# Optimization experiments

Hardware: AMD Instinct MI355X
Metric: run time of the kernel (lower is better)

## Reference

```python
import jax, jax.numpy as jnp
import numpy as np

D = 256
H = 4
HD = D // H


def rotate_half(x):
    xp = x.reshape(x.shape[:-1] + (-1, 2))
    x1, x2 = xp[..., 0], xp[..., 1]
    return jnp.stack((-x2, x1), axis=-1).reshape(x.shape)


def apply_rope(freqs, t):
    # freqs: [2, B, 1, N, HD]; t: [B, H, N, HD]
    return t * freqs[0] + rotate_half(t) * freqs[1]


def layernorm(x, g, b, eps=1e-5):
    m = jnp.mean(x, axis=-1, keepdims=True)
    v = jnp.var(x, axis=-1, keepdims=True)
    return (x - m) * jax.lax.rsqrt(v + eps) * g + b


def ffn(z, W1, b1, g, be, W2, b2):
    h = layernorm(z @ W1 + b1, g, be)
    h = jax.nn.gelu(h, approximate=False)
    return h @ W2 + b2


def heads_split(t):
    B, N, _ = t.shape
    return t.reshape(B, N, H, HD).transpose(0, 2, 1, 3)  # [B,H,N,HD]


def heads_merge(t):
    B, h, N, hd = t.shape
    return t.transpose(0, 2, 1, 3).reshape(B, N, h * hd)


def sdpa(q, k, v):
    s = q.shape[-1] ** (-0.5)
    sim = jnp.einsum('bhid,bhjd->bhij', q, k) * s
    attn = jax.nn.softmax(sim, axis=-1)
    return jnp.einsum('bhij,bhjd->bhid', attn, v)


def self_block(x, enc, Wqkv, bqkv, Wo, bo, W1, b1, g, be, W2, b2):
    B, N, _ = x.shape
    qkv = (x @ Wqkv + bqkv).reshape(B, N, H, HD, 3).transpose(0, 2, 1, 3, 4)
    q, k, v = qkv[..., 0], qkv[..., 1], qkv[..., 2]
    q = apply_rope(enc, q)
    k = apply_rope(enc, k)
    msg = heads_merge(sdpa(q, k, v)) @ Wo + bo
    return x + ffn(jnp.concatenate([x, msg], axis=-1), W1, b1, g, be, W2, b2)


def cross_block(x0, x1, Wqk, bqk, Wv, bv, Wo, bo, W1, b1, g, be, W2, b2):
    qk0 = heads_split(x0 @ Wqk + bqk)
    qk1 = heads_split(x1 @ Wqk + bqk)
    v0 = heads_split(x0 @ Wv + bv)
    v1 = heads_split(x1 @ Wv + bv)
    s = HD ** (-0.5)
    qk0 = qk0 * (s ** 0.5)
    qk1 = qk1 * (s ** 0.5)
    sim = jnp.einsum('bhid,bhjd->bhij', qk0, qk1)
    attn01 = jax.nn.softmax(sim, axis=-1)
    attn10 = jax.nn.softmax(sim.transpose(0, 1, 3, 2), axis=-1)
    m0 = jnp.einsum('bhij,bhjd->bhid', attn01, v1)
    m1 = jnp.einsum('bhij,bhjd->bhid', attn10, v0)
    m0 = heads_merge(m0) @ Wo + bo
    m1 = heads_merge(m1) @ Wo + bo
    x0 = x0 + ffn(jnp.concatenate([x0, m0], axis=-1), W1, b1, g, be, W2, b2)
    x1 = x1 + ffn(jnp.concatenate([x1, m1], axis=-1), W1, b1, g, be, W2, b2)
    return x0, x1


def setup_inputs() -> dict:
    key = jax.random.key(0)
    ks = jax.random.split(key, 24)
    B, N = 4, 2048
    desc0 = jax.random.normal(ks[0], (B, N, D), jnp.float32)
    desc1 = jax.random.normal(ks[1], (B, N, D), jnp.float32)
    encoding0 = jax.random.uniform(ks[2], (2, B, 1, N, HD), jnp.float32)
    encoding1 = jax.random.uniform(ks[3], (2, B, 1, N, HD), jnp.float32)

    def lin(k, fin, fout):
        k1, k2 = jax.random.split(k)
        W = jax.random.normal(k1, (fin, fout), jnp.float32) * (fin ** -0.5)
        b = jax.random.normal(k2, (fout,), jnp.float32) * 0.01
        return W, b

    Wqkv, bqkv = lin(ks[4], D, 3 * D)
    Wo_s, bo_s = lin(ks[5], D, D)
    W1_s, b1_s = lin(ks[6], 2 * D, 2 * D)
    g_s = jnp.ones((2 * D,), jnp.float32)
    be_s = jnp.zeros((2 * D,), jnp.float32)
    W2_s, b2_s = lin(ks[7], 2 * D, D)
    Wqk_c, bqk_c = lin(ks[8], D, D)
    Wv_c, bv_c = lin(ks[9], D, D)
    Wo_c, bo_c = lin(ks[10], D, D)
    W1_c, b1_c = lin(ks[11], 2 * D, 2 * D)
    g_c = jnp.ones((2 * D,), jnp.float32)
    be_c = jnp.zeros((2 * D,), jnp.float32)
    W2_c, b2_c = lin(ks[12], 2 * D, D)
    return dict(desc0=desc0, desc1=desc1, encoding0=encoding0, encoding1=encoding1,
                Wqkv=Wqkv, bqkv=bqkv, Wo_s=Wo_s, bo_s=bo_s,
                W1_s=W1_s, b1_s=b1_s, g_s=g_s, be_s=be_s, W2_s=W2_s, b2_s=b2_s,
                Wqk_c=Wqk_c, bqk_c=bqk_c, Wv_c=Wv_c, bv_c=bv_c, Wo_c=Wo_c, bo_c=bo_c,
                W1_c=W1_c, b1_c=b1_c, g_c=g_c, be_c=be_c, W2_c=W2_c, b2_c=b2_c)


def reference(desc0, desc1, encoding0, encoding1,
              Wqkv, bqkv, Wo_s, bo_s, W1_s, b1_s, g_s, be_s, W2_s, b2_s,
              Wqk_c, bqk_c, Wv_c, bv_c, Wo_c, bo_c, W1_c, b1_c, g_c, be_c, W2_c, b2_c):
    d0 = self_block(desc0, encoding0, Wqkv, bqkv, Wo_s, bo_s, W1_s, b1_s, g_s, be_s, W2_s, b2_s)
    d1 = self_block(desc1, encoding1, Wqkv, bqkv, Wo_s, bo_s, W1_s, b1_s, g_s, be_s, W2_s, b2_s)
    return cross_block(d0, d1, Wqk_c, bqk_c, Wv_c, bv_c, Wo_c, bo_c, W1_c, b1_c, g_c, be_c, W2_c, b2_c)
```

## Files before the change

kernel.cpp:

```cpp
#include <hip/hip_runtime.h>
#include <math.h>

#define BB 4
#define HH 4
#define NN 2048
#define DD 256
#define HDIM 64
#define NTOK 8192
#define NTOK2 16384

typedef __attribute__((ext_vector_type(8))) __bf16 bf16x8;
typedef __attribute__((ext_vector_type(8))) unsigned short ushort8;
typedef __attribute__((ext_vector_type(4))) float floatx4;
typedef __attribute__((ext_vector_type(4))) short short4v;

union U8 { ushort8 u; bf16x8 b; };
union U4 { unsigned int u[2]; unsigned long long l; short4v s; };

#define MFMA16(a, b, c) __builtin_amdgcn_mfma_f32_16x16x16bf16_1k(a, b, c, 0, 0, 0)

__device__ __forceinline__ unsigned short f2bf(float x) {
    unsigned int u = __float_as_uint(x);
    u += 0x7FFF + ((u >> 16) & 1);
    return (unsigned short)(u >> 16);
}
__device__ __forceinline__ float bf2f(unsigned short u) {
    return __uint_as_float(((unsigned int)u) << 16);
}
__device__ __forceinline__ unsigned int pkbf(float a, float b) {
    return ((__float_as_uint(a) + 0x8000u) >> 16) |
           ((__float_as_uint(b) + 0x8000u) & 0xFFFF0000u);
}

struct WTab {
    const float* w[7];
    unsigned short* o[7];
    int K[7];
    int N[7];
    int st[7];
    int t0[8];
};

__global__ __launch_bounds__(256) void wtrans(WTab tab)
{
    __shared__ float lds[32][33];
    const int t = threadIdx.x;
    int bid = blockIdx.x;
    int s = 0;
    while (bid >= tab.t0[s + 1]) s++;
    const int ti = bid - tab.t0[s];
    const int K = tab.K[s], N = tab.N[s], st = tab.st[s];
    const int tx = ti % (N / 32), ty = ti / (N / 32);
    const int k0 = ty * 32, n0 = tx * 32;
    const float* W = tab.w[s];
    unsigned short* Wt = tab.o[s];

    {
        int r = t >> 3, c = (t & 7) * 4;
        float4 a = *(const float4*)&W[(size_t)(k0 + r) * N + n0 + c];
        lds[r][c] = a.x; lds[r][c+1] = a.y; lds[r][c+2] = a.z; lds[r][c+3] = a.w;
    }
    __syncthreads();
    {
        int n = t >> 3, kq = (t & 7) * 4;
        ushort4 p;
        p.x = f2bf(lds[kq+0][n]); p.y = f2bf(lds[kq+1][n]);
        p.z = f2bf(lds[kq+2][n]); p.w = f2bf(lds[kq+3][n]);
        *(ushort4*)&Wt[(size_t)(n0 + n) * st + k0 + kq] = p;
    }
}

__global__ __launch_bounds__(256) void wfuse(
    const float* __restrict__ Wo_s, const float* __restrict__ W1_s,
    unsigned short* __restrict__ o_s,
    const float* __restrict__ Wo_c, const float* __restrict__ W1_c,
    unsigned short* __restrict__ o_c)
{
    __shared__ float wo[32][33];
    __shared__ float w1[32][68];
    const int t = threadIdx.x;
    const int bid = blockIdx.x;
    const int seg = bid >> 6, ti_ = bid & 63;
    const int i0 = (ti_ >> 3) * 32, n0 = (ti_ & 7) * 64;
    const float* Wo  = seg ? Wo_c : Wo_s;
    const float* W1b = (seg ? W1_c : W1_s) + 256 * 512;
    unsigned short* out = seg ? o_c : o_s;
    const int ti = t >> 3, tn = t & 7;

    float acc[8] = {};
    for (int jc = 0; jc < 256; jc += 32) {
        {
            int r = t >> 3, c = (t & 7) * 4;
            *(float4*)&wo[r][c] = *(const float4*)&Wo[(size_t)(i0 + r) * 256 + jc + c];
            int c8 = (t & 7) * 8;
            *(float4*)&w1[r][c8]     = *(const float4*)&W1b[(size_t)(jc + r) * 512 + n0 + c8];
            *(float4*)&w1[r][c8 + 4] = *(const float4*)&W1b[(size_t)(jc + r) * 512 + n0 + c8 + 4];
        }
        __syncthreads();
        #pragma unroll
        for (int j = 0; j < 32; j++) {
            float a = wo[ti][j];
            #pragma unroll
            for (int e = 0; e < 8; e++) acc[e] += a * w1[j][tn * 8 + e];
        }
        __syncthreads();
    }
    #pragma unroll
    for (int e = 0; e < 8; e++)
        out[(size_t)(n0 + tn * 8 + e) * 512 + 256 + i0 + ti] = f2bf(acc[e]);
}

__global__ __launch_bounds__(256) void bfuse(
    const float* bo_s, const float* W1_s, const float* b1_s, float* bs,
    const float* bo_c, const float* W1_c, const float* b1_c, float* bc)
{
    const int seg = blockIdx.x >> 1, half = blockIdx.x & 1;
    const int n = half * 256 + threadIdx.x;
    const float* bo  = seg ? bo_c : bo_s;
    const float* W1b = (seg ? W1_c : W1_s) + 256 * 512;
    const float* b1  = seg ? b1_c : b1_s;
    float* out       = seg ? bc : bs;
    float a = b1[n];
    for (int j = 0; j < 256; j++) a += bo[j] * W1b[(size_t)j * 512 + n];
    out[n] = a;
}

__global__ __launch_bounds__(256) void gemm_mfma(
    const unsigned short* __restrict__ A, int lda,
    const unsigned short* __restrict__ Wt, int K,
    const float* __restrict__ bias, const float* __restrict__ bias2, int mode,
    float* outF, unsigned short* outH0, unsigned short* outH1,
    unsigned short* outH2,
    int ldc, const float* R0, const float* R1)
{
    __shared__ __align__(16) unsigned short As[64 * 40];
    __shared__ __align__(16) unsigned short Bs[128 * 40];
    const int t = threadIdx.x;
    const int w = t >> 6, lane = t & 63, quad = lane >> 4, l15 = lane & 15;
    const int m0 = blockIdx.y * 64, n0 = blockIdx.x * 128;
    const int wn = w * 32;
    const int sar = t >> 2, sac = (t & 3) * 8;
    const int sbr = t >> 1, sbc = (t & 1) * 16;

    const unsigned short* Ap = A  + (size_t)(m0 + sar) * lda + sac;
    const unsigned short* Bp = Wt + (size_t)(n0 + sbr) * K   + sbc;

    ushort8 pa  = *(const ushort8*)(Ap);
    ushort8 pb0 = *(const ushort8*)(Bp);
    ushort8 pb1 = *(const ushort8*)(Bp + 8);

    floatx4 acc[4][2];
    #pragma unroll
    for (int i = 0; i < 4; i++)
        #pragma unroll
        for (int j = 0; j < 2; j++) acc[i][j] = (floatx4){0.f, 0.f, 0.f, 0.f};

    const int nk = K >> 5;
    for (int kk = 0; kk < nk; kk++) {
        *(ushort8*)&As[sar * 40 + sac]     = pa;
        *(ushort8*)&Bs[sbr * 40 + sbc]     = pb0;
        *(ushort8*)&Bs[sbr * 40 + sbc + 8] = pb1;
        __syncthreads();
        if (kk + 1 < nk) {
            int ko = (kk + 1) * 32;
            pa  = *(const ushort8*)(Ap + ko);
            pb0 = *(const ushort8*)(Bp + ko);
            pb1 = *(const ushort8*)(Bp + ko + 8);
        }
        U8 af[4], bf[2];
        #pragma unroll
        for (int i = 0; i < 4; i++)
            af[i].u = *(const ushort8*)&As[(i * 16 + l15) * 40 + quad * 8];
        #pragma unroll
        for (int j = 0; j < 2; j++)
            bf[j].u = *(const ushort8*)&Bs[(wn + j * 16 + l15) * 40 + quad * 8];
        #pragma unroll
        for (int i = 0; i < 4; i++)
            #pragma unroll
            for (int j = 0; j < 2; j++)
                acc[i][j] = __builtin_amdgcn_mfma_f32_16x16x32_bf16(af[i].b, bf[j].b, acc[i][j], 0, 0, 0);
        __syncthreads();
    }

    #pragma unroll
    for (int i = 0; i < 4; i++) {
        #pragma unroll
        for (int j = 0; j < 2; j++) {
            int col = n0 + wn + j * 16 + l15;
            float bv = (mode == 2 && col >= 256) ? bias2[col & 255] : bias[col];
            #pragma unroll
            for (int r = 0; r < 4; r++) {
                int grow = m0 + i * 16 + quad * 4 + r;
                float v = acc[i][j][r] + bv;
                if (mode == 1) {
                    outH0[(size_t)grow * ldc + col] = f2bf(v);
                } else if (mode == 2) {
                    int cc = col & 255;
                    int h = cc >> 6, d = cc & 63;
                    int ds = grow >> 13, b = (grow >> 11) & 3, n = grow & 2047;
                    int bh = ds * 16 + b * 4 + h;
                    if (col < 256)
                        outH0[((size_t)bh * NN + n) * HDIM + d] = f2bf(v);
                    else
                        outH1[((size_t)bh * HDIM + d) * NN + n] = f2bf(v);
                } else if (mode == 3) {
                    int sel = col % 3, cc = col / 3;
                    int h = cc >> 6, d = cc & 63;
                    int ds = grow >> 13, b = (grow >> 11) & 3, n = grow & 2047;
                    int bh = ds * 16 + b * 4 + h;
                    if (sel == 0)
                        outH0[((size_t)bh * NN + n) * HDIM + d] = f2bf(v);
                    else if (sel == 1)
                        outH1[((size_t)bh * NN + n) * HDIM + d] = f2bf(v);
                    else
                        outH2[((size_t)bh * HDIM + d) * NN + n] = f2bf(v);
                } else {
                    const float* R = (grow < NTOK) ? R0 : R1;
                    float vv = v + R[(size_t)(grow & 8191) * 256 + col];
                    outF[(size_t)grow * 256 + col] = vv;
                    if (outH0) outH0[(size_t)grow * 256 + col] = f2bf(vv);
                    if (outH1) outH1[(size_t)grow * 512 + col] = f2bf(vv);
                }
            }
        }
    }
}

__global__ __launch_bounds__(256) void rope_k(unsigned short* __restrict__ qb,
                                              unsigned short* __restrict__ kb,
                                              const float* __restrict__ enc0,
                                              const float* __restrict__ enc1)
{
    int i = blockIdx.x * 256 + threadIdx.x;
    int dp = (i & 31) * 2;
    int n  = (i >> 5) & (NN - 1);
    int h  = (i >> 16) & 3;
    int b  = (i >> 18) & 3;
    int ds = (i >> 20) & 1;
    int bf = (i >> 21) & 1;
    unsigned short* tq = (bf ? kb : qb) +
        (((size_t)(ds * 16 + b * 4 + h)) * NN + n) * HDIM + dp;
    const float* e0 = (ds ? enc1 : enc0) + ((size_t)b * NN + n) * HDIM + dp;
    const float* e1 = e0 + (size_t)BB * NN * HDIM;
    float x0 = bf2f(tq[0]), x1 = bf2f(tq[1]);
    float y0 = x0 * e0[0] - x1 * e1[0];
    float y1 = x1 * e0[1] + x0 * e1[1];
    tq[0] = f2bf(y0); tq[1] = f2bf(y1);
}

__global__ __launch_bounds__(256) void flash_attn(
    const unsigned short* __restrict__ Q, const unsigned short* __restrict__ K,
    const unsigned short* __restrict__ V, unsigned short* __restrict__ O,
    int ldo, int kvx, float qscale)
{
    __shared__ __align__(16) unsigned short Ks[64 * 72];
    __shared__ __align__(16) unsigned short Vt[64 * 72];

    const int t    = threadIdx.x;
    const int w    = t >> 6;
    const int lane = t & 63;
    const int quad = lane >> 4;
    const int l15  = lane & 15;
    const int bh   = blockIdx.y;
    const int kbh  = bh ^ kvx;
    const int q0   = blockIdx.x * 64;

    const unsigned short* Qb  = Q + (size_t)bh  * NN * HDIM;
    const unsigned short* Kb  = K + (size_t)kbh * NN * HDIM;
    const unsigned short* VTb = V + (size_t)kbh * NN * HDIM;

    const int srf = t >> 3, scf = (t & 7) * 8;

    const int qrow = q0 + w * 16 + l15;
    bf16x8 qf0, qf1;
    {
        U8 r0, r1, x0, x1;
        r0.u = *(const ushort8*)&Qb[(size_t)qrow * HDIM + quad * 8];
        r1.u = *(const ushort8*)&Qb[(size_t)qrow * HDIM + 32 + quad * 8];
        #pragma unroll
        for (int j = 0; j < 8; j++) {
            x0.u[j] = f2bf(bf2f(r0.u[j]) * qscale);
            x1.u[j] = f2bf(bf2f(r1.u[j]) * qscale);
        }
        qf0 = x0.b; qf1 = x1.b;
    }

    floatx4 o[4];
    #pragma unroll
    for (int c = 0; c < 4; c++) o[c] = (floatx4){0.f, 0.f, 0.f, 0.f};
    float m = -1e30f, l = 0.f;

    ushort8 ka0 = *(const ushort8*)&Kb[(size_t)srf * HDIM + scf];
    ushort8 ka1 = *(const ushort8*)&Kb[(size_t)(srf + 32) * HDIM + scf];
    ushort8 va0 = *(const ushort8*)&VTb[(size_t)srf * NN + scf];
    ushort8 va1 = *(const ushort8*)&VTb[(size_t)(srf + 32) * NN + scf];

    for (int j0 = 0; j0 < NN; j0 += 64) {
        *(ushort8*)&Ks[srf * 72 + scf]        = ka0;
        *(ushort8*)&Ks[(srf + 32) * 72 + scf] = ka1;
        *(ushort8*)&Vt[srf * 72 + scf]        = va0;
        *(ushort8*)&Vt[(srf + 32) * 72 + scf] = va1;
        __syncthreads();
        if (j0 + 64 < NN) {
            int jn = j0 + 64;
            ka0 = *(const ushort8*)&Kb[(size_t)(jn + srf) * HDIM + scf];
            ka1 = *(const ushort8*)&Kb[(size_t)(jn + srf + 32) * HDIM + scf];
            va0 = *(const ushort8*)&VTb[(size_t)srf * NN + jn + scf];
            va1 = *(const ushort8*)&VTb[(size_t)(srf + 32) * NN + jn + scf];
        }

        floatx4 s[4];
        #pragma unroll
        for (int t4 = 0; t4 < 4; t4++) {
            U8 k0, k1;
            k0.u = *(const ushort8*)&Ks[(t4 * 16 + l15) * 72 + quad * 8];
            k1.u = *(const ushort8*)&Ks[(t4 * 16 + l15) * 72 + 32 + quad * 8];
            floatx4 z = (floatx4){0.f, 0.f, 0.f, 0.f};
            z = __builtin_amdgcn_mfma_f32_16x16x32_bf16(k0.b, qf0, z, 0, 0, 0);
            z = __builtin_amdgcn_mfma_f32_16x16x32_bf16(k1.b, qf1, z, 0, 0, 0);
            s[t4] = z;
        }

        float mx = s[0][0];
        #pragma unroll
        for (int t4 = 0; t4 < 4; t4++)
            #pragma unroll
            for (int r = 0; r < 4; r++) mx = fmaxf(mx, s[t4][r]);
        mx = fmaxf(mx, __shfl_xor(mx, 16, 64));
        mx = fmaxf(mx, __shfl_xor(mx, 32, 64));
        float mn = fmaxf(m, mx);
        float al = exp2f(m - mn);
        m = mn;
        float rs = 0.f;
        #pragma unroll
        for (int t4 = 0; t4 < 4; t4++)
            #pragma unroll
            for (int r = 0; r < 4; r++) {
                float p = exp2f(s[t4][r] - mn);
                s[t4][r] = p;
                rs += p;
            }
        rs += __shfl_xor(rs, 16, 64);
        rs += __shfl_xor(rs, 32, 64);
        l = l * al + rs;
        #pragma unroll
        for (int c = 0; c < 4; c++)
            #pragma unroll
            for (int r = 0; r < 4; r++) o[c][r] *= al;

        short4v pf[4];
        #pragma unroll
        for (int t4 = 0; t4 < 4; t4++) {
            U4 pk;
            pk.u[0] = pkbf(s[t4][0], s[t4][1]);
            pk.u[1] = pkbf(s[t4][2], s[t4][3]);
            pf[t4] = pk.s;
        }

        #pragma unroll
        for (int c = 0; c < 4; c++) {
            #pragma unroll
            for (int t4 = 0; t4 < 4; t4++) {
                U4 vf;
                vf.l = *(const unsigned long long*)
                    &Vt[(c * 16 + l15) * 72 + t4 * 16 + quad * 4];
                o[c] = MFMA16(vf.s, pf[t4], o[c]);
            }
        }
        __syncthreads();
    }

    const int ds = bh >> 4, b = (bh >> 2) & 3, h = bh & 3;
    const int q = q0 + w * 16 + l15;
    const size_t row = (size_t)ds * NTOK + b * NN + q;
    float inv = 1.f / l;
    #pragma unroll
    for (int c = 0; c < 4; c++) {
        ushort4 pk;
        pk.x = f2bf(o[c][0] * inv);
        pk.y = f2bf(o[c][1] * inv);
        pk.z = f2bf(o[c][2] * inv);
        pk.w = f2bf(o[c][3] * inv);
        *(ushort4*)&O[row * ldo + h * HDIM + c * 16 + quad * 4] = pk;
    }
}

__global__ __launch_bounds__(256) void ln_gelu(
    unsigned short* __restrict__ hb, const float* __restrict__ g,
    const float* __restrict__ be)
{
    __shared__ float r1[4], r2[4];
    const int t = threadIdx.x;
    const size_t row = blockIdx.x;
    unsigned short* ip = hb + row * 512;
    float x0 = bf2f(ip[t]), x1 = bf2f(ip[t + 256]);
    float s = x0 + x1, ss = x0 * x0 + x1 * x1;
    #pragma unroll
    for (int o = 32; o > 0; o >>= 1) { s += __shfl_down(s, o); ss += __shfl_down(ss, o); }
    if ((t & 63) == 0) { r1[t >> 6] = s; r2[t >> 6] = ss; }
    __syncthreads();
    float S  = r1[0] + r1[1] + r1[2] + r1[3];
    float SS = r2[0] + r2[1] + r2[2] + r2[3];
    float mean = S * (1.f / 512.f);
    float var  = SS * (1.f / 512.f) - mean * mean;
    float inv  = rsqrtf(var + 1e-5f);
    float y0 = (x0 - mean) * inv * g[t]       + be[t];
    float y1 = (x1 - mean) * inv * g[t + 256] + be[t + 256];
    ip[t]       = f2bf(0.5f * y0 * (1.f + erff(y0 * 0.70710678f)));
    ip[t + 256] = f2bf(0.5f * y1 * (1.f + erff(y1 * 0.70710678f)));
}

__global__ __launch_bounds__(256) void copy_to_cat(
    const float* __restrict__ s0, const float* __restrict__ s1,
    unsigned short* __restrict__ cat)
{
    int i = blockIdx.x * 256 + threadIdx.x;
    int row = i >> 6, c4 = (i & 63) * 4;
    const float* s = (row < NTOK) ? s0 : s1;
    float4 a = *(const float4*)&s[(size_t)(row & 8191) * 256 + c4];
    ushort4 p = { f2bf(a.x), f2bf(a.y), f2bf(a.z), f2bf(a.w) };
    *(ushort4*)&cat[(size_t)row * 512 + c4] = p;
}

extern "C" void kernel_launch(void* const* d_in, const int* in_sizes, int n_in,
                              void* d_out, int out_size, void* d_ws, size_t ws_size,
                              hipStream_t stream)
{
    const float* desc0 = (const float*)d_in[0];
    const float* desc1 = (const float*)d_in[1];
    const float* enc0  = (const float*)d_in[2];
    const float* enc1  = (const float*)d_in[3];
    const float* Wqkv  = (const float*)d_in[4];  const float* bqkv  = (const float*)d_in[5];
    const float* Wo_s  = (const float*)d_in[6];  const float* bo_s  = (const float*)d_in[7];
    const float* W1_s  = (const float*)d_in[8];  const float* b1_s  = (const float*)d_in[9];
    const float* g_s   = (const float*)d_in[10]; const float* be_s  = (const float*)d_in[11];
    const float* W2_s  = (const float*)d_in[12]; const float* b2_s  = (const float*)d_in[13];
    const float* Wqk_c = (const float*)d_in[14]; const float* bqk_c = (const float*)d_in[15];
    const float* Wv_c  = (const float*)d_in[16]; const float* bv_c  = (const float*)d_in[17];
    const float* Wo_c  = (const float*)d_in[18]; const float* bo_c  = (const float*)d_in[19];
    const float* W1_c  = (const float*)d_in[20]; const float* b1_c  = (const float*)d_in[21];
    const float* g_c   = (const float*)d_in[22]; const float* be_c  = (const float*)d_in[23];
    const float* W2_c  = (const float*)d_in[24]; const float* b2_c  = (const float*)d_in[25];

    char* ws = (char*)d_ws;
    unsigned short* wt  = (unsigned short*)ws;
    unsigned short* qb  = (unsigned short*)(ws + 2490368);
    unsigned short* kb  = (unsigned short*)(ws + 10878976);
    unsigned short* vb  = (unsigned short*)(ws + 27656192);
    unsigned short* cat = (unsigned short*)(ws + 36044800);
    unsigned short* hb  = (unsigned short*)(ws + 52822016);
    unsigned short* dbf = (unsigned short*)(ws + 86376448);

    unsigned short* t_qkv  = wt;
    float*          bias_s = (float*)(wt + 196608);
    unsigned short* t_w1s  = wt + 262144;
    unsigned short* t_w2s  = wt + 524288;
    unsigned short* t_wqkc = wt + 655360;
    float*          bias_c = (float*)(wt + 786432);
    unsigned short* t_w1c  = wt + 851968;
    unsigned short* t_w2c  = wt + 1114112;

    float* outF = (float*)d_out;

    dim3 blk(256);

    WTab tab;
    tab.w[0] = Wqkv;  tab.o[0] = t_qkv;          tab.K[0] = 256; tab.N[0] = 768; tab.st[0] = 256;
    tab.w[1] = W1_s;  tab.o[1] = t_w1s;          tab.K[1] = 256; tab.N[1] = 512; tab.st[1] = 512;
    tab.w[2] = W2_s;  tab.o[2] = t_w2s;          tab.K[2] = 512; tab.N[2] = 256; tab.st[2] = 512;
    tab.w[3] = Wqk_c; tab.o[3] = t_wqkc;         tab.K[3] = 256; tab.N[3] = 256; tab.st[3] = 256;
    tab.w[4] = Wv_c;  tab.o[4] = t_wqkc + 65536; tab.K[4] = 256; tab.N[4] = 256; tab.st[4] = 256;
    tab.w[5] = W1_c;  tab.o[5] = t_w1c;          tab.K[5] = 256; tab.N[5] = 512; tab.st[5] = 512;
    tab.w[6] = W2_c;  tab.o[6] = t_w2c;          tab.K[6] = 512; tab.N[6] = 256; tab.st[6] = 512;
    int acc_t = 0;
    for (int s = 0; s < 7; s++) {
        tab.t0[s] = acc_t;
        acc_t += (tab.K[s] / 32) * (tab.N[s] / 32);
    }
    tab.t0[7] = acc_t;
    hipLaunchKernelGGL(wtrans, dim3(acc_t), blk, 0, stream, tab);
    hipLaunchKernelGGL(wfuse, dim3(128), blk, 0, stream,
                       Wo_s, W1_s, t_w1s, Wo_c, W1_c, t_w1c);
    hipLaunchKernelGGL(bfuse, dim3(4), blk, 0, stream,
                       bo_s, W1_s, b1_s, bias_s, bo_c, W1_c, b1_c, bias_c);

    auto gemm = [&](const unsigned short* A, int lda, const unsigned short* Wtp,
                    int K, const float* bias, const float* bias2, int Nc, int mode,
                    float* oF, unsigned short* oh0, unsigned short* oh1,
                    unsigned short* oh2, int ldc, const float* r0, const float* r1) {
        dim3 g(Nc / 128, NTOK2 / 64);
        hipLaunchKernelGGL(gemm_mfma, g, blk, 0, stream,
                           A, lda, Wtp, K, bias, bias2, mode,
                           oF, oh0, oh1, oh2, ldc, r0, r1);
    };

    const float QS = 0.125f * 1.44269504088896f;

    hipLaunchKernelGGL(copy_to_cat, dim3(4096), blk, 0, stream, desc0, desc1, cat);
    gemm(cat, 512, t_qkv, 256, bqkv, nullptr, 768, 3,
         nullptr, qb, kb, vb, 0, nullptr, nullptr);
    hipLaunchKernelGGL(rope_k, dim3(16384), blk, 0, stream, qb, kb, enc0, enc1);
    hipLaunchKernelGGL(flash_attn, dim3(NN / 64, 32), blk, 0, stream,
                       qb, kb, vb, cat + 256, 512, 0, QS);
    gemm(cat, 512, t_w1s, 512, bias_s, nullptr, 512, 1,
         nullptr, hb, nullptr, nullptr, 512, nullptr, nullptr);
    hipLaunchKernelGGL(ln_gelu, dim3(NTOK2), blk, 0, stream, hb, g_s, be_s);
    gemm(hb, 512, t_w2s, 512, b2_s, nullptr, 256, 4,
         outF, dbf, cat, nullptr, 256, desc0, desc1);

    gemm(dbf, 256, t_wqkc, 256, bqk_c, bv_c, 512, 2,
         nullptr, qb, vb, nullptr, 0, nullptr, nullptr);
    hipLaunchKernelGGL(flash_attn, dim3(NN / 64, 32), blk, 0, stream,
                       qb, qb, vb, cat + 256, 512, 16, QS);
    gemm(cat, 512, t_w1c, 512, bias_c, nullptr, 512, 1,
         nullptr, hb, nullptr, nullptr, 512, nullptr, nullptr);
    hipLaunchKernelGGL(ln_gelu, dim3(NTOK2), blk, 0, stream, hb, g_c, be_c);
    gemm(hb, 512, t_w2c, 512, b2_c, nullptr, 256, 4,
         outF, nullptr, nullptr, nullptr, 256, outF, outF + (size_t)NTOK * 256);
}
```

Before: 489.8 us.

## Double-buffer flash attention K/V tiles and process two query tiles per warp

The flash attention kernel now handles 128 query rows per block (32 per warp), so each K/V tile loaded into shared memory feeds twice as many MFMAs. K/V shared buffers are double-buffered, cutting the per-iteration barriers to one. It also adds lazy softmax rescaling (skipped while the running max grows by at most 8), s_setprio around the MFMA phases, and hardware bf16 pack conversion. The trade-offs are higher register pressure and half as many blocks (512 instead of 1024), which lowers parallelism.

```diff
diff --git a/kernel.cpp b/kernel.cpp
--- a/kernel.cpp
+++ b/kernel.cpp
@@ -30,6 +30,17 @@
 __device__ __forceinline__ unsigned int pkbf(float a, float b) {
     return ((__float_as_uint(a) + 0x8000u) >> 16) |
            ((__float_as_uint(b) + 0x8000u) & 0xFFFF0000u);
+}
+__device__ __forceinline__ unsigned int cvtpk(float a, float b) {
+    unsigned int r;
+    asm("v_cvt_pk_bf16_f32 %0, %1, %2" : "=v"(r) : "v"(a), "v"(b));
+    return r;
+}
+__device__ __forceinline__ floatx4 fmax4(floatx4 a, floatx4 b) {
+    floatx4 r;
+    r[0] = fmaxf(a[0], b[0]); r[1] = fmaxf(a[1], b[1]);
+    r[2] = fmaxf(a[2], b[2]); r[3] = fmaxf(a[3], b[3]);
+    return r;
 }
 
 struct WTab {
@@ -253,8 +264,8 @@
     const unsigned short* __restrict__ V, unsigned short* __restrict__ O,
     int ldo, int kvx, float qscale)
 {
-    __shared__ __align__(16) unsigned short Ks[64 * 72];
-    __shared__ __align__(16) unsigned short Vt[64 * 72];
+    __shared__ __align__(16) unsigned short Ks[2][64 * 72];
+    __shared__ __align__(16) unsigned short Vt[2][64 * 72];
 
     const int t    = threadIdx.x;
     const int w    = t >> 6;
@@ -263,7 +274,7 @@
     const int l15  = lane & 15;
     const int bh   = blockIdx.y;
     const int kbh  = bh ^ kvx;
-    const int q0   = blockIdx.x * 64;
+    const int q0   = blockIdx.x * 128;
 
     const unsigned short* Qb  = Q + (size_t)bh  * NN * HDIM;
     const unsigned short* Kb  = K + (size_t)kbh * NN * HDIM;
@@ -271,9 +282,10 @@
 
     const int srf = t >> 3, scf = (t & 7) * 8;
 
-    const int qrow = q0 + w * 16 + l15;
-    bf16x8 qf0, qf1;
-    {
+    bf16x8 qf0[2], qf1[2];
+    #pragma unroll
+    for (int i = 0; i < 2; i++) {
+        const int qrow = q0 + w * 32 + i * 16 + l15;
         U8 r0, r1, x0, x1;
         r0.u = *(const ushort8*)&Qb[(size_t)qrow * HDIM + quad * 8];
         r1.u = *(const ushort8*)&Qb[(size_t)qrow * HDIM + 32 + quad * 8];
@@ -282,106 +294,132 @@
             x0.u[j] = f2bf(bf2f(r0.u[j]) * qscale);
             x1.u[j] = f2bf(bf2f(r1.u[j]) * qscale);
         }
-        qf0 = x0.b; qf1 = x1.b;
-    }
-
-    floatx4 o[4];
-    #pragma unroll
-    for (int c = 0; c < 4; c++) o[c] = (floatx4){0.f, 0.f, 0.f, 0.f};
-    float m = -1e30f, l = 0.f;
+        qf0[i] = x0.b; qf1[i] = x1.b;
+    }
+
+    floatx4 o[2][4];
+    #pragma unroll
+    for (int i = 0; i < 2; i++)
+        #pragma unroll
+        for (int c = 0; c < 4; c++) o[i][c] = (floatx4){0.f, 0.f, 0.f, 0.f};
+    float m[2] = {-1e30f, -1e30f};
+    float l[2] = {0.f, 0.f};
 
     ushort8 ka0 = *(const ushort8*)&Kb[(size_t)srf * HDIM + scf];
     ushort8 ka1 = *(const ushort8*)&Kb[(size_t)(srf + 32) * HDIM + scf];
     ushort8 va0 = *(const ushort8*)&VTb[(size_t)srf * NN + scf];
     ushort8 va1 = *(const ushort8*)&VTb[(size_t)(srf + 32) * NN + scf];
-
-    for (int j0 = 0; j0 < NN; j0 += 64) {
-        *(ushort8*)&Ks[srf * 72 + scf]        = ka0;
-        *(ushort8*)&Ks[(srf + 32) * 72 + scf] = ka1;
-        *(ushort8*)&Vt[srf * 72 + scf]        = va0;
-        *(ushort8*)&Vt[(srf + 32) * 72 + scf] = va1;
-        __syncthreads();
-        if (j0 + 64 < NN) {
-            int jn = j0 + 64;
+    *(ushort8*)&Ks[0][srf * 72 + scf]        = ka0;
+    *(ushort8*)&Ks[0][(srf + 32) * 72 + scf] = ka1;
+    *(ushort8*)&Vt[0][srf * 72 + scf]        = va0;
+    *(ushort8*)&Vt[0][(srf + 32) * 72 + scf] = va1;
+    __syncthreads();
+
+    int cur = 0;
+    for (int j0 = 0; j0 < NN; j0 += 64, cur ^= 1) {
+        const int more = (j0 + 64 < NN);
+        if (more) {
+            const int jn = j0 + 64;
             ka0 = *(const ushort8*)&Kb[(size_t)(jn + srf) * HDIM + scf];
             ka1 = *(const ushort8*)&Kb[(size_t)(jn + srf + 32) * HDIM + scf];
             va0 = *(const ushort8*)&VTb[(size_t)srf * NN + jn + scf];
             va1 = *(const ushort8*)&VTb[(size_t)(srf + 32) * NN + jn + scf];
         }
 
-        floatx4 s[4];
+        floatx4 s[2][4];
+        __builtin_amdgcn_s_setprio(1);
         #pragma unroll
         for (int t4 = 0; t4 < 4; t4++) {
             U8 k0, k1;
-            k0.u = *(const ushort8*)&Ks[(t4 * 16 + l15) * 72 + quad * 8];
-            k1.u = *(const ushort8*)&Ks[(t4 * 16 + l15) * 72 + 32 + quad * 8];
-            floatx4 z = (floatx4){0.f, 0.f, 0.f, 0.f};
-            z = __builtin_amdgcn_mfma_f32_16x16x32_bf16(k0.b, qf0, z, 0, 0, 0);
-            z = __builtin_amdgcn_mfma_f32_16x16x32_bf16(k1.b, qf1, z, 0, 0, 0);
-            s[t4] = z;
-        }
-
-        float mx = s[0][0];
-        #pragma unroll
-        for (int t4 = 0; t4 < 4; t4++)
-            #pragma unroll
-            for (int r = 0; r < 4; r++) mx = fmaxf(mx, s[t4][r]);
-        mx = fmaxf(mx, __shfl_xor(mx, 16, 64));
-        mx = fmaxf(mx, __shfl_xor(mx, 32, 64));
-        float mn = fmaxf(m, mx);
-        float al = exp2f(m - mn);
-        m = mn;
-        float rs = 0.f;
-        #pragma unroll
-        for (int t4 = 0; t4 < 4; t4++)
-            #pragma unroll
-            for (int r = 0; r < 4; r++) {
-                float p = exp2f(s[t4][r] - mn);
-                s[t4][r] = p;
-                rs += p;
+            k0.u = *(const ushort8*)&Ks[cur][(t4 * 16 + l15) * 72 + quad * 8];
+            k1.u = *(const ushort8*)&Ks[cur][(t4 * 16 + l15) * 72 + 32 + quad * 8];
+            #pragma unroll
+            for (int i = 0; i < 2; i++) {
+                floatx4 z = (floatx4){0.f, 0.f, 0.f, 0.f};
+                z = __builtin_amdgcn_mfma_f32_16x16x32_bf16(k0.b, qf0[i], z, 0, 0, 0);
+                z = __builtin_amdgcn_mfma_f32_16x16x32_bf16(k1.b, qf1[i], z, 0, 0, 0);
+                s[i][t4] = z;
             }
-        rs += __shfl_xor(rs, 16, 64);
-        rs += __shfl_xor(rs, 32, 64);
-        l = l * al + rs;
-        #pragma unroll
-        for (int c = 0; c < 4; c++)
-            #pragma unroll
-            for (int r = 0; r < 4; r++) o[c][r] *= al;
-
-        short4v pf[4];
-        #pragma unroll
-        for (int t4 = 0; t4 < 4; t4++) {
+        }
+        __builtin_amdgcn_s_setprio(0);
+
+        short4v pf[2][4];
+        #pragma unroll
+        for (int i = 0; i < 2; i++) {
+            floatx4 a = fmax4(fmax4(s[i][0], s[i][1]), fmax4(s[i][2], s[i][3]));
+            float mx = fmaxf(fmaxf(a[0], a[1]), fmaxf(a[2], a[3]));
+            mx = fmaxf(mx, __shfl_xor(mx, 16, 64));
+            mx = fmaxf(mx, __shfl_xor(mx, 32, 64));
+            if (!__all(mx <= m[i] + 8.f)) {
+                float mn = fmaxf(m[i], mx);
+                float al = exp2f(m[i] - mn);
+                m[i] = mn;
+                l[i] *= al;
+                #pragma unroll
+                for (int c = 0; c < 4; c++)
+                    #pragma unroll
+                    for (int r = 0; r < 4; r++) o[i][c][r] *= al;
+            }
+            float rs = 0.f;
+            #pragma unroll
+            for (int t4 = 0; t4 < 4; t4++)
+                #pragma unroll
+                for (int r = 0; r < 4; r++) {
+                    float p = exp2f(s[i][t4][r] - m[i]);
+                    s[i][t4][r] = p;
+                    rs += p;
+                }
+            rs += __shfl_xor(rs, 16, 64);
+            rs += __shfl_xor(rs, 32, 64);
+            l[i] += rs;
+
+            #pragma unroll
+            for (int t4 = 0; t4 < 4; t4++) {
+                U4 pk;
+                pk.u[0] = cvtpk(s[i][t4][0], s[i][t4][1]);
+                pk.u[1] = cvtpk(s[i][t4][2], s[i][t4][3]);
+                pf[i][t4] = pk.s;
+            }
+        }
+
+        __builtin_amdgcn_s_setprio(1);
+        #pragma unroll
+        for (int c = 0; c < 4; c++) {
+            U4 vf[4];
+            #pragma unroll
+            for (int t4 = 0; t4 < 4; t4++)
+                vf[t4].l = *(const unsigned long long*)
+                    &Vt[cur][(c * 16 + l15) * 72 + t4 * 16 + quad * 4];
+            #pragma unroll
+            for (int i = 0; i < 2; i++)
+                #pragma unroll
+                for (int t4 = 0; t4 < 4; t4++)
+                    o[i][c] = MFMA16(vf[t4].s, pf[i][t4], o[i][c]);
+        }
+        __builtin_amdgcn_s_setprio(0);
+
+        if (more) {
+            *(ushort8*)&Ks[cur ^ 1][srf * 72 + scf]        = ka0;
+            *(ushort8*)&Ks[cur ^ 1][(srf + 32) * 72 + scf] = ka1;
+            *(ushort8*)&Vt[cur ^ 1][srf * 72 + scf]        = va0;
+            *(ushort8*)&Vt[cur ^ 1][(srf + 32) * 72 + scf] = va1;
+            __syncthreads();
+        }
+    }
+
+    const int ds = bh >> 4, b = (bh >> 2) & 3, h = bh & 3;
+    #pragma unroll
+    for (int i = 0; i < 2; i++) {
+        const int q = q0 + w * 32 + i * 16 + l15;
+        const size_t row = (size_t)ds * NTOK + b * NN + q;
+        float inv = 1.f / l[i];
+        #pragma unroll
+        for (int c = 0; c < 4; c++) {
             U4 pk;
-            pk.u[0] = pkbf(s[t4][0], s[t4][1]);
-            pk.u[1] = pkbf(s[t4][2], s[t4][3]);
-            pf[t4] = pk.s;
-        }
-
-        #pragma unroll
-        for (int c = 0; c < 4; c++) {
-            #pragma unroll
-            for (int t4 = 0; t4 < 4; t4++) {
-                U4 vf;
-                vf.l = *(const unsigned long long*)
-                    &Vt[(c * 16 + l15) * 72 + t4 * 16 + quad * 4];
-                o[c] = MFMA16(vf.s, pf[t4], o[c]);
-            }
-        }
-        __syncthreads();
-    }
-
-    const int ds = bh >> 4, b = (bh >> 2) & 3, h = bh & 3;
-    const int q = q0 + w * 16 + l15;
-    const size_t row = (size_t)ds * NTOK + b * NN + q;
-    float inv = 1.f / l;
-    #pragma unroll
-    for (int c = 0; c < 4; c++) {
-        ushort4 pk;
-        pk.x = f2bf(o[c][0] * inv);
-        pk.y = f2bf(o[c][1] * inv);
-        pk.z = f2bf(o[c][2] * inv);
-        pk.w = f2bf(o[c][3] * inv);
-        *(ushort4*)&O[row * ldo + h * HDIM + c * 16 + quad * 4] = pk;
+            pk.u[0] = cvtpk(o[i][c][0] * inv, o[i][c][1] * inv);
+            pk.u[1] = cvtpk(o[i][c][2] * inv, o[i][c][3] * inv);
+            *(unsigned long long*)&O[row * ldo + h * HDIM + c * 16 + quad * 4] = pk.l;
+        }
     }
 }
 
@@ -500,7 +538,7 @@
     gemm(cat, 512, t_qkv, 256, bqkv, nullptr, 768, 3,
          nullptr, qb, kb, vb, 0, nullptr, nullptr);
     hipLaunchKernelGGL(rope_k, dim3(16384), blk, 0, stream, qb, kb, enc0, enc1);
-    hipLaunchKernelGGL(flash_attn, dim3(NN / 64, 32), blk, 0, stream,
+    hipLaunchKernelGGL(flash_attn, dim3(NN / 128, 32), blk, 0, stream,
                        qb, kb, vb, cat + 256, 512, 0, QS);
     gemm(cat, 512, t_w1s, 512, bias_s, nullptr, 512, 1,
          nullptr, hb, nullptr, nullptr, 512, nullptr, nullptr);
@@ -510,7 +548,7 @@
 
     gemm(dbf, 256, t_wqkc, 256, bqk_c, bv_c, 512, 2,
          nullptr, qb, vb, nullptr, 0, nullptr, nullptr);
-    hipLaunchKernelGGL(flash_attn, dim3(NN / 64, 32), blk, 0, stream,
+    hipLaunchKernelGGL(flash_attn, dim3(NN / 128, 32), blk, 0, stream,
                        qb, qb, vb, cat + 256, 512, 16, QS);
     gemm(cat, 512, t_w1c, 512, bias_c, nullptr, 512, 1,
          nullptr, hb, nullptr, nullptr, 512, nullptr, nullptr);
```

New measurement: 486.6 us. No clear change (-0.6%).
